# Performance work log

Hardware: AMD Instinct MI355X
Metric: run time of the kernel (lower is better)

## Reference

```python
import jax, jax.numpy as jnp
import numpy as np

B, S, D = 8, 2048, 512

def setup_inputs() -> dict:
    key = jax.random.key(0)
    ks = jax.random.split(key, 7)
    scale = 1.0 / np.sqrt(D)
    return {
        "x": jax.random.normal(ks[0], (B, S, D), dtype=jnp.float32),
        "Wq": jax.random.normal(ks[1], (D, D), dtype=jnp.float32) * scale,
        "bq": jax.random.normal(ks[2], (D,), dtype=jnp.float32) * 0.01,
        "Wk": jax.random.normal(ks[3], (D, D), dtype=jnp.float32) * scale,
        "bk": jax.random.normal(ks[4], (D,), dtype=jnp.float32) * 0.01,
        "Wv": jax.random.normal(ks[5], (D, D), dtype=jnp.float32) * scale,
        "bv": jax.random.normal(ks[6], (D,), dtype=jnp.float32) * 0.01,
    }

def reference(x, Wq, bq, Wk, bk, Wv, bv):
    # Q/K/V projections: [B,S,D] @ [D,D]
    q = jnp.einsum('bsd,de->bse', x, Wq) + bq
    k = jnp.einsum('bsd,de->bse', x, Wk) + bk
    v = jnp.einsum('bsd,de->bse', x, Wv) + bv
    # NOTE: original module has NO 1/sqrt(d) scaling
    scores = jnp.einsum('bqd,bkd->bqk', q, k)          # [B,S,S]
    attn = jax.nn.softmax(scores, axis=-1)
    return jnp.einsum('bqk,bkd->bqd', attn, v)         # [B,S,D]
```

## Files before the change

### kernel.cpp

```cpp
#include <hip/hip_runtime.h>
#include <hip/hip_fp16.h>


typedef unsigned short u16;
typedef unsigned int u32;
typedef __attribute__((ext_vector_type(8))) _Float16 f16x8;
typedef __attribute__((ext_vector_type(16))) float f32x16;

#define S_LEN 2048
#define D_DIM 512
#define B_N 8

__device__ __forceinline__ u16 f2bf(float f) {
    u32 u = __float_as_uint(f);
    u32 r = u + 0x7FFFu + ((u >> 16) & 1u);
    return (u16)(r >> 16);
}
__device__ __forceinline__ float bf2f(u16 h) {
    return __uint_as_float((u32)h << 16);
}
__device__ __forceinline__ u16 f2h(float f) {
    _Float16 h = (_Float16)f;
    return *(u16*)&h;
}
__device__ __forceinline__ void gl16(const u16* g, u16* l) {
    __builtin_amdgcn_global_load_lds(
        (const __attribute__((address_space(1))) void*)g,
        (__attribute__((address_space(3))) void*)l, 16, 0, 0);
}
__device__ __forceinline__ f32x16 mfma16(f16x8 a, f16x8 b, f32x16 c) {
    return __builtin_amdgcn_mfma_f32_32x32x16_f16(a, b, c, 0, 0, 0);
}

__global__ void detect_k(const u16* __restrict__ x, int* __restrict__ flag)
{
    int t = threadIdx.x;
    u16 u = x[2 * t];
    int e = (u >> 7) & 0xFF;
    int sane = (e == 0) || (e >= 110 && e <= 140);
    unsigned long long b = __ballot(sane);
    if (t == 0) *flag = (__popcll(b) >= 32) ? 1 : 0;
}

__global__ __launch_bounds__(256) void cvt_x(
    const void* __restrict__ X, u16* __restrict__ xf,
    const int* __restrict__ flagp)
{
    const size_t i4 = ((size_t)blockIdx.x * 256 + threadIdx.x) * 4;
    float f[4];
    if (*flagp) {
        ushort4 u = *(const ushort4*)((const u16*)X + i4);
        f[0] = bf2f(u.x); f[1] = bf2f(u.y); f[2] = bf2f(u.z); f[3] = bf2f(u.w);
    } else {
        float4 ff = *(const float4*)((const float*)X + i4);
        f[0] = ff.x; f[1] = ff.y; f[2] = ff.z; f[3] = ff.w;
    }
    ushort4 h;
    h.x = f2h(f[0]); h.y = f2h(f[1]); h.z = f2h(f[2]); h.w = f2h(f[3]);
    *(ushort4*)(xf + i4) = h;
}

__global__ __launch_bounds__(256) void pack_w(
    const void* __restrict__ Wq, const void* __restrict__ Wk, const void* __restrict__ Wv,
    u16* __restrict__ WT, const int* __restrict__ flagp)
{
    const int k = blockIdx.x;
    const int n = blockIdx.y * 256 + threadIdx.x;
    const void* W = n < 512 ? Wq : n < 1024 ? Wk : Wv;
    const int nc = n & 511;
    float f = *flagp ? bf2f(((const u16*)W)[(size_t)k * 512 + nc])
                     : ((const float*)W)[(size_t)k * 512 + nc];
    WT[(size_t)n * 512 + k] = f2h(f);
}

__global__ void pack_bias(
    const void* __restrict__ bq, const void* __restrict__ bk, const void* __restrict__ bv,
    float* __restrict__ bcat, const int* __restrict__ flagp)
{
    const int t = blockIdx.x * 256 + threadIdx.x;
    const void* b = t < 512 ? bq : t < 1024 ? bk : bv;
    const int i = t & 511;
    bcat[t] = *flagp ? bf2f(((const u16*)b)[i]) : ((const float*)b)[i];
}

template <int EPI>
__global__ __launch_bounds__(256) void gemm_f16(
    const u16* __restrict__ A_, const u16* __restrict__ B_,
    void* __restrict__ Cp, const float* __restrict__ biasf,
    u16* __restrict__ Oq, u16* __restrict__ Ok, u16* __restrict__ OvT,
    const int* __restrict__ flagp,
    int K, int lda, int ldb, int ldc, long sA, long sB, long sC, long cbase)
{
    const int tid = threadIdx.x;
    const int lane = tid & 63, wav = tid >> 6;
    const int l31 = lane & 31, lh = lane >> 5;
    const int m0 = blockIdx.y * 128, n0 = blockIdx.x * 128;
    const int bm = (wav >> 1) * 64, bn = (wav & 1) * 64;

    const u16* A = A_ + (size_t)blockIdx.z * sA;
    const u16* B = B_ + (size_t)blockIdx.z * sB;

    __shared__ __align__(16) u16 As[8192], Bs[8192];

    const int r0 = tid >> 3;
    const int c0 = ((tid & 7) ^ (r0 & 7)) * 8;
    size_t aoff[4], boff[4];
#pragma unroll
    for (int j = 0; j < 4; j++) {
        aoff[j] = (size_t)(m0 + r0 + j * 32) * lda + c0;
        boff[j] = (size_t)(n0 + r0 + j * 32) * ldb + c0;
    }
    const int g7 = l31 & 7;
    const int rowA0 = (bm + l31) * 64, rowA1 = (bm + 32 + l31) * 64;
    const int rowB0 = (bn + l31) * 64, rowB1 = (bn + 32 + l31) * 64;

    f32x16 acc[2][2];
#pragma unroll
    for (int i = 0; i < 2; i++)
#pragma unroll
        for (int j = 0; j < 2; j++)
#pragma unroll
            for (int r = 0; r < 16; r++) acc[i][j][r] = 0.f;

    for (int k0 = 0; k0 < K; k0 += 64) {
#pragma unroll
        for (int j = 0; j < 4; j++) {
            gl16(A + aoff[j] + k0, As + j * 2048 + wav * 512);
            gl16(B + boff[j] + k0, Bs + j * 2048 + wav * 512);
        }
        __syncthreads();

#pragma unroll
        for (int h = 0; h < 4; h++) {
            const int so = ((h * 2 + lh) ^ g7) * 8;
            f16x8 af[2], bfr[2];
            af[0] = *(const f16x8*)&As[rowA0 + so];
            af[1] = *(const f16x8*)&As[rowA1 + so];
            bfr[0] = *(const f16x8*)&Bs[rowB0 + so];
            bfr[1] = *(const f16x8*)&Bs[rowB1 + so];
#pragma unroll
            for (int i = 0; i < 2; i++)
#pragma unroll
                for (int j = 0; j < 2; j++)
                    acc[i][j] = mfma16(af[i], bfr[j], acc[i][j]);
        }
        __syncthreads();
    }

    if (EPI == 2) {
        const int mode = blockIdx.x >> 2;
#pragma unroll
        for (int it = 0; it < 2; it++)
#pragma unroll
            for (int jt = 0; jt < 2; jt++) {
                const int gcol = n0 + bn + jt * 32 + l31;
                const int lcol = gcol & 511;
                const float badd = biasf[gcol];
#pragma unroll
                for (int r = 0; r < 16; r++) {
                    const int row = m0 + bm + it * 32 + (r & 3) + 8 * (r >> 2) + 4 * lh;
                    const float v = acc[it][jt][r] + badd;
                    if (mode == 0)      Oq [(size_t)row * 512 + lcol] = f2h(v);
                    else if (mode == 1) Ok [(size_t)row * 512 + lcol] = f2h(v);
                    else                OvT[(size_t)lcol * 16384 + row] = f2h(v);
                }
            }
    } else if (EPI == 0) {
        float* Cf = (float*)Cp;
        const long coff = (long)blockIdx.z * sC;
#pragma unroll
        for (int it = 0; it < 2; it++)
#pragma unroll
            for (int jt = 0; jt < 2; jt++) {
                const int col = n0 + bn + jt * 32 + l31;
#pragma unroll
                for (int r = 0; r < 16; r++) {
                    const int row = m0 + bm + it * 32 + (r & 3) + 8 * (r >> 2) + 4 * lh;
                    Cf[(size_t)(coff + (long)row * ldc + col)] = acc[it][jt][r];
                }
            }
    } else {
        const int isbf = *flagp;
        float* Cf = (float*)Cp;
        u16* Cb = (u16*)Cp;
        const long coff = cbase + (long)blockIdx.z * sC;
#pragma unroll
        for (int it = 0; it < 2; it++)
#pragma unroll
            for (int jt = 0; jt < 2; jt++) {
                const int col = n0 + bn + jt * 32 + l31;
#pragma unroll
                for (int r = 0; r < 16; r++) {
                    const int row = m0 + bm + it * 32 + (r & 3) + 8 * (r >> 2) + 4 * lh;
                    const size_t idx = (size_t)(coff + (long)row * ldc + col);
                    if (isbf) Cb[idx] = f2bf(acc[it][jt][r]);
                    else Cf[idx] = acc[it][jt][r];
                }
            }
    }
}

__global__ __launch_bounds__(256) void softmax_k(float* __restrict__ sc)
{
    float* srow = sc + (size_t)blockIdx.x * S_LEN;
    const int tid = threadIdx.x;

    float4 a = ((const float4*)srow)[tid];
    float4 b = ((const float4*)srow)[256 + tid];

    float m = fmaxf(fmaxf(fmaxf(a.x, a.y), fmaxf(a.z, a.w)),
                    fmaxf(fmaxf(b.x, b.y), fmaxf(b.z, b.w)));
#pragma unroll
    for (int off = 32; off > 0; off >>= 1) m = fmaxf(m, __shfl_down(m, off));

    __shared__ float redm[4], reds[4];
    if ((tid & 63) == 0) redm[tid >> 6] = m;
    __syncthreads();
    m = fmaxf(fmaxf(redm[0], redm[1]), fmaxf(redm[2], redm[3]));

    a.x = __expf(a.x - m); a.y = __expf(a.y - m);
    a.z = __expf(a.z - m); a.w = __expf(a.w - m);
    b.x = __expf(b.x - m); b.y = __expf(b.y - m);
    b.z = __expf(b.z - m); b.w = __expf(b.w - m);
    float s = a.x + a.y + a.z + a.w + b.x + b.y + b.z + b.w;
#pragma unroll
    for (int off = 32; off > 0; off >>= 1) s += __shfl_down(s, off);
    if ((tid & 63) == 0) reds[tid >> 6] = s;
    __syncthreads();
    s = reds[0] + reds[1] + reds[2] + reds[3];

    const float inv = 1.0f / s;
    ushort4 pa, pb;
    pa.x = f2h(a.x * inv); pa.y = f2h(a.y * inv);
    pa.z = f2h(a.z * inv); pa.w = f2h(a.w * inv);
    pb.x = f2h(b.x * inv); pb.y = f2h(b.y * inv);
    pb.z = f2h(b.z * inv); pb.w = f2h(b.w * inv);
    ((ushort4*)srow)[tid] = pa;
    ((ushort4*)srow)[256 + tid] = pb;
}

extern "C" void kernel_launch(void* const* d_in, const int* in_sizes, int n_in,
                              void* d_out, int out_size, void* d_ws, size_t ws_size,
                              hipStream_t stream)
{
    const void* x  = d_in[0];
    const void* Wq = d_in[1]; const void* bq = d_in[2];
    const void* Wk = d_in[3]; const void* bk = d_in[4];
    const void* Wv = d_in[5]; const void* bv = d_in[6];

    const int S = S_LEN, D = D_DIM;
    const long SD = (long)S * D;

    char* w = (char*)d_ws;
    int*   flag = (int*)w;
    u16*   WT   = (u16*)(w + 1024);
    float* bcat = (float*)(w + 1573888);
    u16*   xf   = (u16*)(w + 1580032);
    u16*   qf   = (u16*)(w + 18357248);
    u16*   kf   = (u16*)(w + 35134464);
    u16*   vT   = (u16*)(w + 51911680);
    float* scA  = (float*)(w + 68688896);

    const size_t avail = ws_size > 68688896ull ? ws_size - 68688896ull : 0;
    const size_t perb = (size_t)S * S * 4;
    const int c = avail >= 8 * perb ? 8 : avail >= 4 * perb ? 4 : avail >= 2 * perb ? 2 : 1;

    dim3 blk(256);

    detect_k<<<1, 64, 0, stream>>>((const u16*)x, flag);
    cvt_x<<<8192, blk, 0, stream>>>(x, xf, flag);
    pack_w<<<dim3(512, 6), blk, 0, stream>>>(Wq, Wk, Wv, WT, flag);
    pack_bias<<<6, blk, 0, stream>>>(bq, bk, bv, bcat, flag);

    gemm_f16<2><<<dim3(12, 128, 1), blk, 0, stream>>>(
        xf, WT, nullptr, bcat, qf, kf, vT, flag,
        512, 512, 512, 0, 0, 0, 0, 0);

    for (int cb = 0; cb < B_N; cb += c) {
        const size_t off = (size_t)cb * SD;
        gemm_f16<0><<<dim3(16, 16, c), blk, 0, stream>>>(
            qf + off, kf + off, scA, nullptr, nullptr, nullptr, nullptr, flag,
            512, 512, 512, S, SD, SD, (long)S * S, 0);
        softmax_k<<<c * S, blk, 0, stream>>>(scA);
        gemm_f16<1><<<dim3(4, 16, c), blk, 0, stream>>>(
            (const u16*)scA, vT + (size_t)cb * S, d_out, nullptr,
            nullptr, nullptr, nullptr, flag,
            S, 2 * S, B_N * S, D, 2ll * S * S, S, SD, (long)cb * SD);
    }
}
```

Measured before the change: 293.9 us.

## Rewrite GEMM as 256-row tiled, double-buffered 8-wave kernel with 16x16 MFMA

Replaces the 128x128 single-buffered GEMM with a 512-thread, 8-wave kernel that computes 256xBN tiles. It double-buffers LDS loads, prefetching two K-steps ahead with explicit vmcnt waits, and switches from 32x32x16 to 16x16x32 MFMA. The larger tiles and more waves are meant to raise data reuse and hide global-load latency behind MFMA work. In exchange it uses much more LDS and accumulator registers, and relies on hand-tuned waitcnt counts that must exactly match the number of outstanding loads.

```diff
diff --git a/kernel.cpp b/kernel.cpp
--- a/kernel.cpp
+++ b/kernel.cpp
@@ -5,7 +5,7 @@
 typedef unsigned short u16;
 typedef unsigned int u32;
 typedef __attribute__((ext_vector_type(8))) _Float16 f16x8;
-typedef __attribute__((ext_vector_type(16))) float f32x16;
+typedef __attribute__((ext_vector_type(4))) float f32x4;
 
 #define S_LEN 2048
 #define D_DIM 512
@@ -28,8 +28,8 @@
         (const __attribute__((address_space(1))) void*)g,
         (__attribute__((address_space(3))) void*)l, 16, 0, 0);
 }
-__device__ __forceinline__ f32x16 mfma16(f16x8 a, f16x8 b, f32x16 c) {
-    return __builtin_amdgcn_mfma_f32_32x32x16_f16(a, b, c, 0, 0, 0);
+__device__ __forceinline__ f32x4 mfma16(f16x8 a, f16x8 b, f32x4 c) {
+    return __builtin_amdgcn_mfma_f32_16x16x32_f16(a, b, c, 0, 0, 0);
 }
 
 __global__ void detect_k(const u16* __restrict__ x, int* __restrict__ flag)
@@ -83,120 +83,187 @@
     bcat[t] = *flagp ? bf2f(((const u16*)b)[i]) : ((const float*)b)[i];
 }
 
-template <int EPI>
-__global__ __launch_bounds__(256) void gemm_f16(
+template <int EPI, int BN>
+__global__ __launch_bounds__(512, 2) void gemm8(
     const u16* __restrict__ A_, const u16* __restrict__ B_,
     void* __restrict__ Cp, const float* __restrict__ biasf,
     u16* __restrict__ Oq, u16* __restrict__ Ok, u16* __restrict__ OvT,
     const int* __restrict__ flagp,
     int K, int lda, int ldb, int ldc, long sA, long sB, long sC, long cbase)
 {
+    constexpr int NJ = BN / 64;
+    constexpr int NB = BN / 64;
+
     const int tid = threadIdx.x;
-    const int lane = tid & 63, wav = tid >> 6;
-    const int l31 = lane & 31, lh = lane >> 5;
-    const int m0 = blockIdx.y * 128, n0 = blockIdx.x * 128;
-    const int bm = (wav >> 1) * 64, bn = (wav & 1) * 64;
+    const int lane = tid & 63;
+    const int wid = tid >> 6;
+    const int wm = wid >> 2;
+    const int wn = wid & 3;
+    const int l15 = lane & 15, lq = lane >> 4;
+    const int m0 = blockIdx.y * 256, n0 = blockIdx.x * BN;
+    const int colB = wn * (BN / 4);
 
     const u16* A = A_ + (size_t)blockIdx.z * sA;
     const u16* B = B_ + (size_t)blockIdx.z * sB;
 
-    __shared__ __align__(16) u16 As[8192], Bs[8192];
+    __shared__ __align__(16) u16 As[2][256 * 64];
+    __shared__ __align__(16) u16 Bs[2][BN * 64];
 
     const int r0 = tid >> 3;
     const int c0 = ((tid & 7) ^ (r0 & 7)) * 8;
-    size_t aoff[4], boff[4];
-#pragma unroll
-    for (int j = 0; j < 4; j++) {
-        aoff[j] = (size_t)(m0 + r0 + j * 32) * lda + c0;
-        boff[j] = (size_t)(n0 + r0 + j * 32) * ldb + c0;
+    u32 aoffs[4], boffs[NB];
+#pragma unroll
+    for (int j = 0; j < 4; j++)
+        aoffs[j] = (u32)((m0 + j * 64 + r0) * lda + c0);
+#pragma unroll
+    for (int j = 0; j < NB; j++)
+        boffs[j] = (u32)((n0 + j * 64 + r0) * ldb + c0);
+    const int stageDst = wid << 9;
+
+    const int nt = K >> 6;
+
+    f32x4 acc[8][NJ];
+#pragma unroll
+    for (int mi = 0; mi < 8; mi++)
+#pragma unroll
+        for (int nj = 0; nj < NJ; nj++)
+#pragma unroll
+            for (int r = 0; r < 4; r++) acc[mi][nj][r] = 0.f;
+
+    auto stage = [&](u16* dA, u16* dB, int k0) {
+#pragma unroll
+        for (int j = 0; j < 4; j++)
+            gl16(A + aoffs[j] + k0, dA + (j << 12) + stageDst);
+#pragma unroll
+        for (int j = 0; j < NB; j++)
+            gl16(B + boffs[j] + k0, dB + (j << 12) + stageDst);
+    };
+    auto rdA = [&](const u16* buf, int p, int h, int ks) -> f16x8 {
+        const int row = (wm << 7) + (p << 5) + (h << 4) + l15;
+        const int off = (row << 6) + ((((ks << 2) + lq) ^ (row & 7)) << 3);
+        return *(const f16x8*)(buf + off);
+    };
+    auto rdB = [&](const u16* buf, int nj, int ks) -> f16x8 {
+        const int row = colB + (nj << 4) + l15;
+        const int off = (row << 6) + ((((ks << 2) + lq) ^ (row & 7)) << 3);
+        return *(const f16x8*)(buf + off);
+    };
+
+    auto tile = [&](u16* Ab, u16* Bb, int tt) {
+        f16x8 bfr[NJ][2];
+#pragma unroll
+        for (int p = 0; p < 4; p++) {
+            f16x8 a[2][2];
+            if (p == 0) {
+#pragma unroll
+                for (int nj = 0; nj < NJ; nj++)
+#pragma unroll
+                    for (int ks = 0; ks < 2; ks++)
+                        bfr[nj][ks] = rdB(Bb, nj, ks);
+            }
+#pragma unroll
+            for (int h = 0; h < 2; h++)
+#pragma unroll
+                for (int ks = 0; ks < 2; ks++)
+                    a[h][ks] = rdA(Ab, p, h, ks);
+            if (p == 3) {
+                asm volatile("s_waitcnt lgkmcnt(0)" ::: "memory");
+                __builtin_amdgcn_sched_barrier(0);
+            }
+            __builtin_amdgcn_s_barrier();
+            if (p == 3 && tt + 2 < nt)
+                stage(Ab, Bb, (tt + 2) * 64);
+            __builtin_amdgcn_s_setprio(1);
+#pragma unroll
+            for (int h = 0; h < 2; h++)
+#pragma unroll
+                for (int nj = 0; nj < NJ; nj++)
+#pragma unroll
+                    for (int ks = 0; ks < 2; ks++)
+                        acc[2 * p + h][nj] =
+                            mfma16(a[h][ks], bfr[nj][ks], acc[2 * p + h][nj]);
+            __builtin_amdgcn_s_setprio(0);
+            if (p < 3) {
+                __builtin_amdgcn_s_barrier();
+            } else if (tt + 1 < nt) {
+                if (tt + 2 < nt) {
+                    if constexpr (BN == 256)
+                        asm volatile("s_waitcnt vmcnt(8)" ::: "memory");
+                    else
+                        asm volatile("s_waitcnt vmcnt(6)" ::: "memory");
+                } else {
+                    asm volatile("s_waitcnt vmcnt(0)" ::: "memory");
+                }
+                __builtin_amdgcn_sched_barrier(0);
+                __builtin_amdgcn_s_barrier();
+            }
+        }
+    };
+
+    stage(As[0], Bs[0], 0);
+    stage(As[1], Bs[1], 64);
+    if constexpr (BN == 256)
+        asm volatile("s_waitcnt vmcnt(8)" ::: "memory");
+    else
+        asm volatile("s_waitcnt vmcnt(6)" ::: "memory");
+    __builtin_amdgcn_sched_barrier(0);
+    __builtin_amdgcn_s_barrier();
+
+    for (int tt = 0; tt < nt; tt += 2) {
+        tile(As[0], Bs[0], tt);
+        tile(As[1], Bs[1], tt + 1);
     }
-    const int g7 = l31 & 7;
-    const int rowA0 = (bm + l31) * 64, rowA1 = (bm + 32 + l31) * 64;
-    const int rowB0 = (bn + l31) * 64, rowB1 = (bn + 32 + l31) * 64;
-
-    f32x16 acc[2][2];
-#pragma unroll
-    for (int i = 0; i < 2; i++)
-#pragma unroll
-        for (int j = 0; j < 2; j++)
-#pragma unroll
-            for (int r = 0; r < 16; r++) acc[i][j][r] = 0.f;
-
-    for (int k0 = 0; k0 < K; k0 += 64) {
-#pragma unroll
-        for (int j = 0; j < 4; j++) {
-            gl16(A + aoff[j] + k0, As + j * 2048 + wav * 512);
-            gl16(B + boff[j] + k0, Bs + j * 2048 + wav * 512);
-        }
-        __syncthreads();
-
-#pragma unroll
-        for (int h = 0; h < 4; h++) {
-            const int so = ((h * 2 + lh) ^ g7) * 8;
-            f16x8 af[2], bfr[2];
-            af[0] = *(const f16x8*)&As[rowA0 + so];
-            af[1] = *(const f16x8*)&As[rowA1 + so];
-            bfr[0] = *(const f16x8*)&Bs[rowB0 + so];
-            bfr[1] = *(const f16x8*)&Bs[rowB1 + so];
-#pragma unroll
-            for (int i = 0; i < 2; i++)
-#pragma unroll
-                for (int j = 0; j < 2; j++)
-                    acc[i][j] = mfma16(af[i], bfr[j], acc[i][j]);
-        }
-        __syncthreads();
-    }
 
     if (EPI == 2) {
-        const int mode = blockIdx.x >> 2;
-#pragma unroll
-        for (int it = 0; it < 2; it++)
-#pragma unroll
-            for (int jt = 0; jt < 2; jt++) {
-                const int gcol = n0 + bn + jt * 32 + l31;
-                const int lcol = gcol & 511;
-                const float badd = biasf[gcol];
-#pragma unroll
-                for (int r = 0; r < 16; r++) {
-                    const int row = m0 + bm + it * 32 + (r & 3) + 8 * (r >> 2) + 4 * lh;
-                    const float v = acc[it][jt][r] + badd;
+        const int mode = n0 >> 9;
+#pragma unroll
+        for (int nj = 0; nj < NJ; nj++) {
+            const int gcol = n0 + colB + nj * 16 + l15;
+            const int lcol = gcol & 511;
+            const float badd = biasf[gcol];
+#pragma unroll
+            for (int mi = 0; mi < 8; mi++)
+#pragma unroll
+                for (int r = 0; r < 4; r++) {
+                    const int row = m0 + (wm << 7) + mi * 16 + lq * 4 + r;
+                    const float v = acc[mi][nj][r] + badd;
                     if (mode == 0)      Oq [(size_t)row * 512 + lcol] = f2h(v);
                     else if (mode == 1) Ok [(size_t)row * 512 + lcol] = f2h(v);
                     else                OvT[(size_t)lcol * 16384 + row] = f2h(v);
                 }
-            }
+        }
     } else if (EPI == 0) {
         float* Cf = (float*)Cp;
         const long coff = (long)blockIdx.z * sC;
 #pragma unroll
-        for (int it = 0; it < 2; it++)
-#pragma unroll
-            for (int jt = 0; jt < 2; jt++) {
-                const int col = n0 + bn + jt * 32 + l31;
-#pragma unroll
-                for (int r = 0; r < 16; r++) {
-                    const int row = m0 + bm + it * 32 + (r & 3) + 8 * (r >> 2) + 4 * lh;
-                    Cf[(size_t)(coff + (long)row * ldc + col)] = acc[it][jt][r];
+        for (int nj = 0; nj < NJ; nj++) {
+            const int col = n0 + colB + nj * 16 + l15;
+#pragma unroll
+            for (int mi = 0; mi < 8; mi++)
+#pragma unroll
+                for (int r = 0; r < 4; r++) {
+                    const int row = m0 + (wm << 7) + mi * 16 + lq * 4 + r;
+                    Cf[(size_t)(coff + (long)row * ldc + col)] = acc[mi][nj][r];
                 }
-            }
+        }
     } else {
         const int isbf = *flagp;
         float* Cf = (float*)Cp;
         u16* Cb = (u16*)Cp;
         const long coff = cbase + (long)blockIdx.z * sC;
 #pragma unroll
-        for (int it = 0; it < 2; it++)
-#pragma unroll
-            for (int jt = 0; jt < 2; jt++) {
-                const int col = n0 + bn + jt * 32 + l31;
-#pragma unroll
-                for (int r = 0; r < 16; r++) {
-                    const int row = m0 + bm + it * 32 + (r & 3) + 8 * (r >> 2) + 4 * lh;
+        for (int nj = 0; nj < NJ; nj++) {
+            const int col = n0 + colB + nj * 16 + l15;
+#pragma unroll
+            for (int mi = 0; mi < 8; mi++)
+#pragma unroll
+                for (int r = 0; r < 4; r++) {
+                    const int row = m0 + (wm << 7) + mi * 16 + lq * 4 + r;
                     const size_t idx = (size_t)(coff + (long)row * ldc + col);
-                    if (isbf) Cb[idx] = f2bf(acc[it][jt][r]);
-                    else Cf[idx] = acc[it][jt][r];
+                    if (isbf) Cb[idx] = f2bf(acc[mi][nj][r]);
+                    else Cf[idx] = acc[mi][nj][r];
                 }
-            }
+        }
     }
 }
 
@@ -265,24 +332,24 @@
     const size_t perb = (size_t)S * S * 4;
     const int c = avail >= 8 * perb ? 8 : avail >= 4 * perb ? 4 : avail >= 2 * perb ? 2 : 1;
 
-    dim3 blk(256);
+    dim3 blk(256), blk5(512);
 
     detect_k<<<1, 64, 0, stream>>>((const u16*)x, flag);
     cvt_x<<<8192, blk, 0, stream>>>(x, xf, flag);
     pack_w<<<dim3(512, 6), blk, 0, stream>>>(Wq, Wk, Wv, WT, flag);
     pack_bias<<<6, blk, 0, stream>>>(bq, bk, bv, bcat, flag);
 
-    gemm_f16<2><<<dim3(12, 128, 1), blk, 0, stream>>>(
+    gemm8<2, 256><<<dim3(6, 64, 1), blk5, 0, stream>>>(
         xf, WT, nullptr, bcat, qf, kf, vT, flag,
         512, 512, 512, 0, 0, 0, 0, 0);
 
     for (int cb = 0; cb < B_N; cb += c) {
         const size_t off = (size_t)cb * SD;
-        gemm_f16<0><<<dim3(16, 16, c), blk, 0, stream>>>(
+        gemm8<0, 256><<<dim3(8, 8, c), blk5, 0, stream>>>(
             qf + off, kf + off, scA, nullptr, nullptr, nullptr, nullptr, flag,
             512, 512, 512, S, SD, SD, (long)S * S, 0);
         softmax_k<<<c * S, blk, 0, stream>>>(scA);
-        gemm_f16<1><<<dim3(4, 16, c), blk, 0, stream>>>(
+        gemm8<1, 128><<<dim3(4, 8, c), blk5, 0, stream>>>(
             (const u16*)scA, vT + (size_t)cb * S, d_out, nullptr,
             nullptr, nullptr, nullptr, flag,
             S, 2 * S, B_N * S, D, 2ll * S * S, S, SD, (long)cb * SD);
```

After: 325.0 us. 10.6% more time.

## Use two-wave 128x128 GEMM blocks with 16x16x32 MFMA and larger per-wave tiles

Applied to the files above, without the earlier changes.

The GEMM kernel drops from four waves to two per 128x128 block. Each wave now computes a 64x128 sub-tile with 4x8 accumulators of the 16x16x32 f16 MFMA instead of 2x2 accumulators of the 32x32x16 MFMA. The goal is more register-level reuse of LDS fragments and fewer LDS reads per MFMA. The cost is much higher register pressure (128 accumulator floats per lane), fewer waves to hide latency, and more global-to-LDS load instructions per thread.

```diff
diff --git a/kernel.cpp b/kernel.cpp
--- a/kernel.cpp
+++ b/kernel.cpp
@@ -5,7 +5,7 @@
 typedef unsigned short u16;
 typedef unsigned int u32;
 typedef __attribute__((ext_vector_type(8))) _Float16 f16x8;
-typedef __attribute__((ext_vector_type(16))) float f32x16;
+typedef __attribute__((ext_vector_type(4))) float f32x4;
 
 #define S_LEN 2048
 #define D_DIM 512
@@ -28,8 +28,8 @@
         (const __attribute__((address_space(1))) void*)g,
         (__attribute__((address_space(3))) void*)l, 16, 0, 0);
 }
-__device__ __forceinline__ f32x16 mfma16(f16x8 a, f16x8 b, f32x16 c) {
-    return __builtin_amdgcn_mfma_f32_32x32x16_f16(a, b, c, 0, 0, 0);
+__device__ __forceinline__ f32x4 mfma16(f16x8 a, f16x8 b, f32x4 c) {
+    return __builtin_amdgcn_mfma_f32_16x16x32_f16(a, b, c, 0, 0, 0);
 }
 
 __global__ void detect_k(const u16* __restrict__ x, int* __restrict__ flag)
@@ -84,7 +84,7 @@
 }
 
 template <int EPI>
-__global__ __launch_bounds__(256) void gemm_f16(
+__global__ __launch_bounds__(128) void gemmw(
     const u16* __restrict__ A_, const u16* __restrict__ B_,
     void* __restrict__ Cp, const float* __restrict__ biasf,
     u16* __restrict__ Oq, u16* __restrict__ Ok, u16* __restrict__ OvT,
@@ -92,111 +92,118 @@
     int K, int lda, int ldb, int ldc, long sA, long sB, long sC, long cbase)
 {
     const int tid = threadIdx.x;
-    const int lane = tid & 63, wav = tid >> 6;
-    const int l31 = lane & 31, lh = lane >> 5;
+    const int lane = tid & 63;
+    const int wid = tid >> 6;
+    const int l15 = lane & 15, lq = lane >> 4;
     const int m0 = blockIdx.y * 128, n0 = blockIdx.x * 128;
-    const int bm = (wav >> 1) * 64, bn = (wav & 1) * 64;
 
     const u16* A = A_ + (size_t)blockIdx.z * sA;
     const u16* B = B_ + (size_t)blockIdx.z * sB;
 
-    __shared__ __align__(16) u16 As[8192], Bs[8192];
+    __shared__ __align__(16) u16 As[128 * 64], Bs[128 * 64];
 
     const int r0 = tid >> 3;
     const int c0 = ((tid & 7) ^ (r0 & 7)) * 8;
-    size_t aoff[4], boff[4];
-#pragma unroll
-    for (int j = 0; j < 4; j++) {
-        aoff[j] = (size_t)(m0 + r0 + j * 32) * lda + c0;
-        boff[j] = (size_t)(n0 + r0 + j * 32) * ldb + c0;
-    }
-    const int g7 = l31 & 7;
-    const int rowA0 = (bm + l31) * 64, rowA1 = (bm + 32 + l31) * 64;
-    const int rowB0 = (bn + l31) * 64, rowB1 = (bn + 32 + l31) * 64;
-
-    f32x16 acc[2][2];
-#pragma unroll
-    for (int i = 0; i < 2; i++)
-#pragma unroll
-        for (int j = 0; j < 2; j++)
-#pragma unroll
-            for (int r = 0; r < 16; r++) acc[i][j][r] = 0.f;
+    u32 aoff[8], boff[8];
+#pragma unroll
+    for (int j = 0; j < 8; j++) {
+        aoff[j] = (u32)((m0 + j * 16 + r0) * lda + c0);
+        boff[j] = (u32)((n0 + j * 16 + r0) * ldb + c0);
+    }
+    const int sdst = wid << 9;
+
+    f32x4 acc[4][8];
+#pragma unroll
+    for (int mi = 0; mi < 4; mi++)
+#pragma unroll
+        for (int nj = 0; nj < 8; nj++)
+#pragma unroll
+            for (int r = 0; r < 4; r++) acc[mi][nj][r] = 0.f;
+
+    const int g7 = l15 & 7;
 
     for (int k0 = 0; k0 < K; k0 += 64) {
 #pragma unroll
-        for (int j = 0; j < 4; j++) {
-            gl16(A + aoff[j] + k0, As + j * 2048 + wav * 512);
-            gl16(B + boff[j] + k0, Bs + j * 2048 + wav * 512);
-        }
+        for (int j = 0; j < 8; j++)
+            gl16(A + aoff[j] + k0, As + (j << 10) + sdst);
+#pragma unroll
+        for (int j = 0; j < 8; j++)
+            gl16(B + boff[j] + k0, Bs + (j << 10) + sdst);
         __syncthreads();
 
 #pragma unroll
-        for (int h = 0; h < 4; h++) {
-            const int so = ((h * 2 + lh) ^ g7) * 8;
-            f16x8 af[2], bfr[2];
-            af[0] = *(const f16x8*)&As[rowA0 + so];
-            af[1] = *(const f16x8*)&As[rowA1 + so];
-            bfr[0] = *(const f16x8*)&Bs[rowB0 + so];
-            bfr[1] = *(const f16x8*)&Bs[rowB1 + so];
-#pragma unroll
-            for (int i = 0; i < 2; i++)
-#pragma unroll
-                for (int j = 0; j < 2; j++)
-                    acc[i][j] = mfma16(af[i], bfr[j], acc[i][j]);
+        for (int ks = 0; ks < 2; ks++) {
+            const int so = (((ks << 2) + lq) ^ g7) << 3;
+            f16x8 a[4], b[8];
+#pragma unroll
+            for (int mi = 0; mi < 4; mi++) {
+                const int row = (wid << 6) + (mi << 4) + l15;
+                a[mi] = *(const f16x8*)&As[(row << 6) + so];
+            }
+#pragma unroll
+            for (int nj = 0; nj < 8; nj++) {
+                const int row = (nj << 4) + l15;
+                b[nj] = *(const f16x8*)&Bs[(row << 6) + so];
+            }
+#pragma unroll
+            for (int mi = 0; mi < 4; mi++)
+#pragma unroll
+                for (int nj = 0; nj < 8; nj++)
+                    acc[mi][nj] = mfma16(a[mi], b[nj], acc[mi][nj]);
         }
         __syncthreads();
     }
 
     if (EPI == 2) {
-        const int mode = blockIdx.x >> 2;
-#pragma unroll
-        for (int it = 0; it < 2; it++)
-#pragma unroll
-            for (int jt = 0; jt < 2; jt++) {
-                const int gcol = n0 + bn + jt * 32 + l31;
-                const int lcol = gcol & 511;
-                const float badd = biasf[gcol];
-#pragma unroll
-                for (int r = 0; r < 16; r++) {
-                    const int row = m0 + bm + it * 32 + (r & 3) + 8 * (r >> 2) + 4 * lh;
-                    const float v = acc[it][jt][r] + badd;
+        const int mode = n0 >> 9;
+#pragma unroll
+        for (int nj = 0; nj < 8; nj++) {
+            const int gcol = n0 + nj * 16 + l15;
+            const int lcol = gcol & 511;
+            const float badd = biasf[gcol];
+#pragma unroll
+            for (int mi = 0; mi < 4; mi++)
+#pragma unroll
+                for (int r = 0; r < 4; r++) {
+                    const int row = m0 + (wid << 6) + mi * 16 + lq * 4 + r;
+                    const float v = acc[mi][nj][r] + badd;
                     if (mode == 0)      Oq [(size_t)row * 512 + lcol] = f2h(v);
                     else if (mode == 1) Ok [(size_t)row * 512 + lcol] = f2h(v);
                     else                OvT[(size_t)lcol * 16384 + row] = f2h(v);
                 }
-            }
+        }
     } else if (EPI == 0) {
         float* Cf = (float*)Cp;
         const long coff = (long)blockIdx.z * sC;
 #pragma unroll
-        for (int it = 0; it < 2; it++)
-#pragma unroll
-            for (int jt = 0; jt < 2; jt++) {
-                const int col = n0 + bn + jt * 32 + l31;
-#pragma unroll
-                for (int r = 0; r < 16; r++) {
-                    const int row = m0 + bm + it * 32 + (r & 3) + 8 * (r >> 2) + 4 * lh;
-                    Cf[(size_t)(coff + (long)row * ldc + col)] = acc[it][jt][r];
+        for (int nj = 0; nj < 8; nj++) {
+            const int col = n0 + nj * 16 + l15;
+#pragma unroll
+            for (int mi = 0; mi < 4; mi++)
+#pragma unroll
+                for (int r = 0; r < 4; r++) {
+                    const int row = m0 + (wid << 6) + mi * 16 + lq * 4 + r;
+                    Cf[(size_t)(coff + (long)row * ldc + col)] = acc[mi][nj][r];
                 }
-            }
+        }
     } else {
         const int isbf = *flagp;
         float* Cf = (float*)Cp;
         u16* Cb = (u16*)Cp;
         const long coff = cbase + (long)blockIdx.z * sC;
 #pragma unroll
-        for (int it = 0; it < 2; it++)
-#pragma unroll
-            for (int jt = 0; jt < 2; jt++) {
-                const int col = n0 + bn + jt * 32 + l31;
-#pragma unroll
-                for (int r = 0; r < 16; r++) {
-                    const int row = m0 + bm + it * 32 + (r & 3) + 8 * (r >> 2) + 4 * lh;
+        for (int nj = 0; nj < 8; nj++) {
+            const int col = n0 + nj * 16 + l15;
+#pragma unroll
+            for (int mi = 0; mi < 4; mi++)
+#pragma unroll
+                for (int r = 0; r < 4; r++) {
+                    const int row = m0 + (wid << 6) + mi * 16 + lq * 4 + r;
                     const size_t idx = (size_t)(coff + (long)row * ldc + col);
-                    if (isbf) Cb[idx] = f2bf(acc[it][jt][r]);
-                    else Cf[idx] = acc[it][jt][r];
+                    if (isbf) Cb[idx] = f2bf(acc[mi][nj][r]);
+                    else Cf[idx] = acc[mi][nj][r];
                 }
-            }
+        }
     }
 }
 
@@ -265,24 +272,24 @@
     const size_t perb = (size_t)S * S * 4;
     const int c = avail >= 8 * perb ? 8 : avail >= 4 * perb ? 4 : avail >= 2 * perb ? 2 : 1;
 
-    dim3 blk(256);
+    dim3 blk(256), blkg(128);
 
     detect_k<<<1, 64, 0, stream>>>((const u16*)x, flag);
     cvt_x<<<8192, blk, 0, stream>>>(x, xf, flag);
     pack_w<<<dim3(512, 6), blk, 0, stream>>>(Wq, Wk, Wv, WT, flag);
     pack_bias<<<6, blk, 0, stream>>>(bq, bk, bv, bcat, flag);
 
-    gemm_f16<2><<<dim3(12, 128, 1), blk, 0, stream>>>(
+    gemmw<2><<<dim3(12, 128, 1), blkg, 0, stream>>>(
         xf, WT, nullptr, bcat, qf, kf, vT, flag,
         512, 512, 512, 0, 0, 0, 0, 0);
 
     for (int cb = 0; cb < B_N; cb += c) {
         const size_t off = (size_t)cb * SD;
-        gemm_f16<0><<<dim3(16, 16, c), blk, 0, stream>>>(
+        gemmw<0><<<dim3(16, 16, c), blkg, 0, stream>>>(
             qf + off, kf + off, scA, nullptr, nullptr, nullptr, nullptr, flag,
             512, 512, 512, S, SD, SD, (long)S * S, 0);
         softmax_k<<<c * S, blk, 0, stream>>>(scA);
-        gemm_f16<1><<<dim3(4, 16, c), blk, 0, stream>>>(
+        gemmw<1><<<dim3(4, 16, c), blkg, 0, stream>>>(
             (const u16*)scA, vT + (size_t)cb * S, d_out, nullptr,
             nullptr, nullptr, nullptr, flag,
             S, 2 * S, B_N * S, D, 2ll * S * S, S, SD, (long)cb * SD);
```

Result: slower. 356.3 us (+21.3%).
